# Kernel optimization log

Hardware: AMD Instinct MI355X
Metric: run time of the kernel (lower is better)

## Reference

```python
import jax, jax.numpy as jnp
import numpy as np

B = 128          # number of graphs
N = 512          # nodes per graph
D = 128          # input_dim == hid_dim
H = 128          # hid_dim
L = 2            # num GIN layers
E_PG = 8192      # edges per graph (avg degree 16)
OUT = 10
BN_EPS = 1e-5
RATIO = 0.5


def setup_inputs() -> dict:
    key = jax.random.key(0)
    ks = jax.random.split(key, 32)
    NT = B * N
    # per-graph random edges, offset into the global node index space
    e = jax.random.randint(ks[0], (2, B, E_PG), 0, N)
    offs = (jnp.arange(B) * N)[None, :, None]
    edge_index = (e + offs).reshape(2, -1).astype(jnp.int64)
    batch = jnp.repeat(jnp.arange(B), N).astype(jnp.int64)
    x = jax.random.normal(ks[1], (NT, D), dtype=jnp.float32)
    sc = 0.05
    inp = {
        'x': x, 'edge_index': edge_index, 'batch': batch,
        'epss': jax.random.normal(ks[2], (L,), jnp.float32) * 0.1,
        'Ws1': jax.random.normal(ks[3], (L, D, 2 * H), jnp.float32) * sc,
        'bs1': jax.random.normal(ks[4], (L, 2 * H), jnp.float32) * sc,
        'g1s': jax.random.uniform(ks[5], (L, 2 * H), jnp.float32, 0.5, 1.5),
        'be1s': jax.random.normal(ks[6], (L, 2 * H), jnp.float32) * sc,
        'rm1s': jax.random.normal(ks[7], (L, 2 * H), jnp.float32) * 0.1,
        'rv1s': jax.random.uniform(ks[8], (L, 2 * H), jnp.float32, 0.5, 1.5),
        'Ws2': jax.random.normal(ks[9], (L, 2 * H, H), jnp.float32) * sc,
        'bs2': jax.random.normal(ks[10], (L, H), jnp.float32) * sc,
        'gbn': jax.random.uniform(ks[11], (L, H), jnp.float32, 0.5, 1.5),
        'bbn': jax.random.normal(ks[12], (L, H), jnp.float32) * sc,
        'rmbn': jax.random.normal(ks[13], (L, H), jnp.float32) * 0.1,
        'rvbn': jax.random.uniform(ks[14], (L, H), jnp.float32, 0.5, 1.5),
        'Wrel': jax.random.normal(ks[15], (H, 1), jnp.float32) * sc,
        'brel': jax.random.normal(ks[16], (1,), jnp.float32) * sc,
        'Wroot': jax.random.normal(ks[17], (H, 1), jnp.float32) * sc,
        'W_lin1': jax.random.normal(ks[18], (H, H), jnp.float32) * sc,
        'b_lin1': jax.random.normal(ks[19], (H,), jnp.float32) * sc,
        'g_h': jax.random.uniform(ks[20], (H,), jnp.float32, 0.5, 1.5),
        'be_h': jax.random.normal(ks[21], (H,), jnp.float32) * sc,
        'rm_h': jax.random.normal(ks[22], (H,), jnp.float32) * 0.1,
        'rv_h': jax.random.uniform(ks[23], (H,), jnp.float32, 0.5, 1.5),
        'W_lin2': jax.random.normal(ks[24], (H, OUT), jnp.float32) * sc,
        'b_lin2': jax.random.normal(ks[25], (OUT,), jnp.float32) * sc,
    }
    return inp


def _bn(h, g, b, rm, rv):
    # eval-mode BatchNorm1d
    return (h - rm) * jax.lax.rsqrt(rv + BN_EPS) * g + b


def _forward(x, edge_index, batch, epss, Ws1, bs1, g1s, be1s, rm1s, rv1s,
             Ws2, bs2, gbn, bbn, rmbn, rvbn, Wrel, brel, Wroot,
             W_lin1, b_lin1, g_h, be_h, rm_h, rv_h, W_lin2, b_lin2):
    NT = x.shape[0]
    src, dst = edge_index[0], edge_index[1]
    # ---- stacked GINConv + BN + ReLU (eval: dropout = identity) ----
    for l in range(L):
        agg = jax.ops.segment_sum(x[src], dst, num_segments=NT)   # scatter-add
        h = (1.0 + epss[l]) * x + agg
        h = h @ Ws1[l] + bs1[l]
        h = jax.nn.relu(_bn(h, g1s[l], be1s[l], rm1s[l], rv1s[l]))
        h = h @ Ws2[l] + bs2[l]
        x = jax.nn.relu(_bn(h, gbn[l], bbn[l], rmbn[l], rvbn[l]))
    # ---- SAGPooling: GraphConv score -> tanh -> per-graph top-k ----
    agg = jax.ops.segment_sum(x[src], dst, num_segments=NT)
    score = (agg @ Wrel + brel + x @ Wroot)[:, 0]                 # [NT]
    s = jnp.tanh(score)
    K = int(np.ceil(RATIO * N))
    vals, idx = jax.lax.top_k(s.reshape(B, N), K)                 # [B,K]
    perm = (idx + (jnp.arange(B) * N)[:, None]).reshape(-1)       # global node ids
    x_pool = x[perm] * vals.reshape(-1)[:, None]                  # [B*K, H]
    batch_pool = batch[perm]
    # ---- global add pool ----
    embedding = jax.ops.segment_sum(x_pool, batch_pool, num_segments=B)  # [B,H]
    # ---- head (B > 1 branch) ----
    h = _bn(embedding @ W_lin1 + b_lin1, g_h, be_h, rm_h, rv_h)
    h = jax.nn.relu(h)
    logits = h @ W_lin2 + b_lin2
    return embedding, logits


def reference(x, edge_index, batch, epss, Ws1, bs1, g1s, be1s, rm1s, rv1s,
              Ws2, bs2, gbn, bbn, rmbn, rvbn, Wrel, brel, Wroot,
              W_lin1, b_lin1, g_h, be_h, rm_h, rv_h, W_lin2, b_lin2):
    return _forward(x, edge_index, batch, epss, Ws1, bs1, g1s, be1s, rm1s,
                    rv1s, Ws2, bs2, gbn, bbn, rmbn, rvbn, Wrel, brel, Wroot,
                    W_lin1, b_lin1, g_h, be_h, rm_h, rv_h, W_lin2, b_lin2)
```

## Files before the change

kernel.cpp:

```cpp
#include <hip/hip_runtime.h>
#include <hip/hip_bf16.h>
#include <stdint.h>
#include <math.h>

#define NT_ 65536
#define BGRAPH 128
#define NNODE 512
#define DIM 128
#define HID 128
#define H2 256
#define EDGES 1048576
#define EPG 8192
#define KSEL 256
#define OUTC 10

typedef float v2f __attribute__((ext_vector_type(2)));

__global__ __launch_bounds__(512) void k_csr(const int* __restrict__ src, const int* __restrict__ dst,
                                             int* __restrict__ row_start, int* __restrict__ csr2) {
    __shared__ int hist[512];
    __shared__ int scan_s[512];
    __shared__ int cur[512];
    __shared__ int eids[EPG];
    const int g = blockIdx.x;
    const int t = threadIdx.x;
    const int base = g * EPG;
    const int nb = g * NNODE;
    hist[t] = 0;
    __syncthreads();
    #pragma unroll
    for (int j = t; j < EPG; j += 512) {
        int d = dst[base + j] - nb;
        atomicAdd(&hist[d], 1);
    }
    __syncthreads();
    int v = hist[t];
    scan_s[t] = v;
    __syncthreads();
    for (int off = 1; off < 512; off <<= 1) {
        int u = (t >= off) ? scan_s[t - off] : 0;
        __syncthreads();
        scan_s[t] += u;
        __syncthreads();
    }
    int excl = scan_s[t] - v;
    row_start[nb + t] = base + excl;
    cur[t] = excl;
    if (g == BGRAPH - 1 && t == 511) row_start[NT_] = EDGES;
    __syncthreads();
    #pragma unroll
    for (int j = t; j < EPG; j += 512) {
        int d = dst[base + j] - nb;
        int pos = atomicAdd(&cur[d], 1);
        eids[pos] = (d << 16) | j;
    }
    __syncthreads();
    #pragma unroll
    for (int p = t; p < EPG; p += 512) {
        int packed = eids[p];
        int j = packed & 0xFFFF;
        int d = packed >> 16;
        int beg = scan_s[d] - hist[d];
        int end = scan_s[d];
        int rank = 0;
        for (int q = beg; q < end; ++q) rank += (int)((eids[q] & 0xFFFF) < j);
        csr2[base + beg + rank] = src[base + j];
    }
}

__global__ __launch_bounds__(256) void k_aggcomb(const float* __restrict__ X,
        const int* __restrict__ row_start, const int* __restrict__ csr_src,
        const float* __restrict__ epss, int l, float* __restrict__ XIN) {
    int bid = blockIdx.x;
    int wg = (bid & 7) * 1024 + (bid >> 3);
    int wave = threadIdx.x >> 6;
    int lane = threadIdx.x & 63;
    int half = lane >> 5;
    int l32 = lane & 31;
    int n = wg * 8 + wave * 2 + half;
    int beg = row_start[n], end = row_start[n + 1];
    const size_t co = (size_t)(l32 * 4);
    const float ep = __fadd_rn(1.0f, epss[l]);
    float a0 = 0.f, a1 = 0.f, a2 = 0.f, a3 = 0.f;
    int p = beg;
    for (; p + 8 <= end; p += 8) {
        int n0 = csr_src[p+0], n1 = csr_src[p+1], n2 = csr_src[p+2], n3 = csr_src[p+3];
        int n4 = csr_src[p+4], n5 = csr_src[p+5], n6 = csr_src[p+6], n7 = csr_src[p+7];
        float4 v0 = *(const float4*)(X + (size_t)n0 * DIM + co);
        float4 v1 = *(const float4*)(X + (size_t)n1 * DIM + co);
        float4 v2 = *(const float4*)(X + (size_t)n2 * DIM + co);
        float4 v3 = *(const float4*)(X + (size_t)n3 * DIM + co);
        float4 v4 = *(const float4*)(X + (size_t)n4 * DIM + co);
        float4 v5 = *(const float4*)(X + (size_t)n5 * DIM + co);
        float4 v6 = *(const float4*)(X + (size_t)n6 * DIM + co);
        float4 v7 = *(const float4*)(X + (size_t)n7 * DIM + co);
        a0 = __fadd_rn(a0, v0.x); a1 = __fadd_rn(a1, v0.y); a2 = __fadd_rn(a2, v0.z); a3 = __fadd_rn(a3, v0.w);
        a0 = __fadd_rn(a0, v1.x); a1 = __fadd_rn(a1, v1.y); a2 = __fadd_rn(a2, v1.z); a3 = __fadd_rn(a3, v1.w);
        a0 = __fadd_rn(a0, v2.x); a1 = __fadd_rn(a1, v2.y); a2 = __fadd_rn(a2, v2.z); a3 = __fadd_rn(a3, v2.w);
        a0 = __fadd_rn(a0, v3.x); a1 = __fadd_rn(a1, v3.y); a2 = __fadd_rn(a2, v3.z); a3 = __fadd_rn(a3, v3.w);
        a0 = __fadd_rn(a0, v4.x); a1 = __fadd_rn(a1, v4.y); a2 = __fadd_rn(a2, v4.z); a3 = __fadd_rn(a3, v4.w);
        a0 = __fadd_rn(a0, v5.x); a1 = __fadd_rn(a1, v5.y); a2 = __fadd_rn(a2, v5.z); a3 = __fadd_rn(a3, v5.w);
        a0 = __fadd_rn(a0, v6.x); a1 = __fadd_rn(a1, v6.y); a2 = __fadd_rn(a2, v6.z); a3 = __fadd_rn(a3, v6.w);
        a0 = __fadd_rn(a0, v7.x); a1 = __fadd_rn(a1, v7.y); a2 = __fadd_rn(a2, v7.z); a3 = __fadd_rn(a3, v7.w);
    }
    for (; p < end; ++p) {
        int nbr = csr_src[p];
        float4 v = *(const float4*)(X + (size_t)nbr * DIM + co);
        a0 = __fadd_rn(a0, v.x); a1 = __fadd_rn(a1, v.y); a2 = __fadd_rn(a2, v.z); a3 = __fadd_rn(a3, v.w);
    }
    float4 xv = *(const float4*)(X + (size_t)n * DIM + co);
    float4 o;
    o.x = __fadd_rn(__fmul_rn(ep, xv.x), a0);
    o.y = __fadd_rn(__fmul_rn(ep, xv.y), a1);
    o.z = __fadd_rn(__fmul_rn(ep, xv.z), a2);
    o.w = __fadd_rn(__fmul_rn(ep, xv.w), a3);
    *(float4*)(XIN + (size_t)n * DIM + co) = o;
}

__global__ __launch_bounds__(256) void k_gemm1(const float* __restrict__ XIN,
        const float* __restrict__ Ws1, const float* __restrict__ bs1,
        const float* __restrict__ g1s, const float* __restrict__ be1s, const float* __restrict__ rm1s,
        const float* __restrict__ rv1s, int l, float* __restrict__ H1out) {
    __shared__ float As[2][16][132];
    __shared__ float Bs[2][16][132];
    const float* W1  = Ws1 + (size_t)l * DIM * H2;
    const float* b1  = bs1 + l * H2;
    const float* g1  = g1s + l * H2;
    const float* be1 = be1s + l * H2;
    const float* rm1 = rm1s + l * H2;
    const float* rv1 = rv1s + l * H2;
    int bid = blockIdx.x;
    int wg = (bid & 7) * 128 + (bid >> 3);
    const int mbase = (wg >> 1) * 128;
    const int nbase = (wg & 1) * 128;
    const int tid = threadIdx.x;
    const int srow = tid >> 1;
    const int sk   = (tid & 1) * 8;
    const int bk   = tid >> 4;
    const int bc   = (tid & 15) * 4;
    const int ty = tid >> 4;
    const int tx = tid & 15;
    v2f acc[8][4] = {};
    const float* xr = XIN + (size_t)(mbase + srow) * DIM + sk;
    float4 px0, px1, pw0, pw1;
    px0 = *(const float4*)(xr);     px1 = *(const float4*)(xr + 4);
    {
        const float* wrow = W1 + (size_t)bk * H2 + nbase;
        pw0 = *(const float4*)(wrow + bc); pw1 = *(const float4*)(wrow + bc + 64);
    }
    As[0][sk + 0][srow] = px0.x;
    As[0][sk + 1][srow] = px0.y;
    As[0][sk + 2][srow] = px0.z;
    As[0][sk + 3][srow] = px0.w;
    As[0][sk + 4][srow] = px1.x;
    As[0][sk + 5][srow] = px1.y;
    As[0][sk + 6][srow] = px1.z;
    As[0][sk + 7][srow] = px1.w;
    *(float4*)&Bs[0][bk][bc]      = pw0;
    *(float4*)&Bs[0][bk][bc + 64] = pw1;
    __syncthreads();
    int cur = 0;
    for (int kt = 0; kt < DIM; kt += 16) {
        const int nxt = kt + 16;
        if (nxt < DIM) {
            px0 = *(const float4*)(xr + nxt);     px1 = *(const float4*)(xr + nxt + 4);
            const float* wrow = W1 + (size_t)(nxt + bk) * H2 + nbase;
            pw0 = *(const float4*)(wrow + bc); pw1 = *(const float4*)(wrow + bc + 64);
        }
        #pragma unroll
        for (int kk = 0; kk < 16; ++kk) {
            const float4 aA = *(const float4*)&As[cur][kk][ty * 8];
            const float4 aB = *(const float4*)&As[cur][kk][ty * 8 + 4];
            const float4 b0 = *(const float4*)&Bs[cur][kk][tx * 4];
            const float4 b1v = *(const float4*)&Bs[cur][kk][tx * 4 + 64];
            v2f b00; b00[0] = b0.x;  b00[1] = b0.y;
            v2f b01; b01[0] = b0.z;  b01[1] = b0.w;
            v2f b10; b10[0] = b1v.x; b10[1] = b1v.y;
            v2f b11; b11[0] = b1v.z; b11[1] = b1v.w;
            const float arr[8] = {aA.x, aA.y, aA.z, aA.w, aB.x, aB.y, aB.z, aB.w};
            #pragma unroll
            for (int i = 0; i < 8; ++i) {
                v2f ai; ai[0] = arr[i]; ai[1] = arr[i];
                acc[i][0] = __builtin_elementwise_fma(ai, b00, acc[i][0]);
                acc[i][1] = __builtin_elementwise_fma(ai, b01, acc[i][1]);
                acc[i][2] = __builtin_elementwise_fma(ai, b10, acc[i][2]);
                acc[i][3] = __builtin_elementwise_fma(ai, b11, acc[i][3]);
            }
        }
        if (nxt < DIM) {
            const int nb = cur ^ 1;
            As[nb][sk + 0][srow] = px0.x;
            As[nb][sk + 1][srow] = px0.y;
            As[nb][sk + 2][srow] = px0.z;
            As[nb][sk + 3][srow] = px0.w;
            As[nb][sk + 4][srow] = px1.x;
            As[nb][sk + 5][srow] = px1.y;
            As[nb][sk + 6][srow] = px1.z;
            As[nb][sk + 7][srow] = px1.w;
            *(float4*)&Bs[nb][bk][bc]      = pw0;
            *(float4*)&Bs[nb][bk][bc + 64] = pw1;
            __syncthreads();
        }
        cur ^= 1;
    }
    const int gc = nbase + tx * 4;
    float bb[8], iv[8], gg[8], rr[8], ee[8];
    #pragma unroll
    for (int j = 0; j < 8; ++j) {
        int c = (j < 4) ? (gc + j) : (gc + 60 + j);
        bb[j] = b1[c];
        iv[j] = __fdiv_rn(1.0f, __fsqrt_rn(__fadd_rn(rv1[c], 1e-5f)));
        gg[j] = g1[c];
        rr[j] = rm1[c];
        ee[j] = be1[c];
    }
    #pragma unroll
    for (int i = 0; i < 8; ++i) {
        const int gr = mbase + ty * 8 + i;
        float cv[8] = {acc[i][0][0], acc[i][0][1], acc[i][1][0], acc[i][1][1],
                       acc[i][2][0], acc[i][2][1], acc[i][3][0], acc[i][3][1]};
        float r[8];
        #pragma unroll
        for (int j = 0; j < 8; ++j) {
            float t = __fadd_rn(cv[j], bb[j]);
            t = __fsub_rn(t, rr[j]); t = __fmul_rn(t, iv[j]);
            t = __fmul_rn(t, gg[j]); t = __fadd_rn(t, ee[j]);
            r[j] = fmaxf(t, 0.f);
        }
        float4 o0; o0.x = r[0]; o0.y = r[1]; o0.z = r[2]; o0.w = r[3];
        float4 o1; o1.x = r[4]; o1.y = r[5]; o1.z = r[6]; o1.w = r[7];
        *(float4*)(H1out + (size_t)gr * H2 + gc)      = o0;
        *(float4*)(H1out + (size_t)gr * H2 + gc + 64) = o1;
    }
}

__global__ __launch_bounds__(256) void k_gemm2(const float* __restrict__ H1, const float* __restrict__ Ws2,
        const float* __restrict__ bs2, const float* __restrict__ gbn, const float* __restrict__ bbn,
        const float* __restrict__ rmbn, const float* __restrict__ rvbn, int l, float* __restrict__ Xout) {
    __shared__ float As[2][16][132];
    __shared__ float Bs[2][16][132];
    const float* W2 = Ws2 + (size_t)l * H2 * HID;
    const float* b2 = bs2 + l * HID;
    const float* g  = gbn + l * HID;
    const float* be = bbn + l * HID;
    const float* rm = rmbn + l * HID;
    const float* rv = rvbn + l * HID;
    int bid = blockIdx.x;
    int wg = (bid & 7) * 64 + (bid >> 3);
    const int mbase = wg * 128;
    const int tid = threadIdx.x;
    const int srow = tid >> 1;
    const int sk   = (tid & 1) * 8;
    const int bk   = tid >> 4;
    const int bc   = (tid & 15) * 4;
    const int ty = tid >> 4;
    const int tx = tid & 15;
    v2f acc[8][4] = {};
    const float* hr = H1 + (size_t)(mbase + srow) * H2 + sk;
    float4 ph0, ph1, pw0, pw1;
    ph0 = *(const float4*)(hr);     ph1 = *(const float4*)(hr + 4);
    {
        const float* wrow = W2 + (size_t)bk * HID;
        pw0 = *(const float4*)(wrow + bc); pw1 = *(const float4*)(wrow + bc + 64);
    }
    As[0][sk + 0][srow] = ph0.x;
    As[0][sk + 1][srow] = ph0.y;
    As[0][sk + 2][srow] = ph0.z;
    As[0][sk + 3][srow] = ph0.w;
    As[0][sk + 4][srow] = ph1.x;
    As[0][sk + 5][srow] = ph1.y;
    As[0][sk + 6][srow] = ph1.z;
    As[0][sk + 7][srow] = ph1.w;
    *(float4*)&Bs[0][bk][bc]      = pw0;
    *(float4*)&Bs[0][bk][bc + 64] = pw1;
    __syncthreads();
    int cur = 0;
    for (int kt = 0; kt < H2; kt += 16) {
        const int nxt = kt + 16;
        if (nxt < H2) {
            ph0 = *(const float4*)(hr + nxt);     ph1 = *(const float4*)(hr + nxt + 4);
            const float* wrow = W2 + (size_t)(nxt + bk) * HID;
            pw0 = *(const float4*)(wrow + bc); pw1 = *(const float4*)(wrow + bc + 64);
        }
        #pragma unroll
        for (int kk = 0; kk < 16; ++kk) {
            const float4 aA = *(const float4*)&As[cur][kk][ty * 8];
            const float4 aB = *(const float4*)&As[cur][kk][ty * 8 + 4];
            const float4 b0 = *(const float4*)&Bs[cur][kk][tx * 4];
            const float4 b1v = *(const float4*)&Bs[cur][kk][tx * 4 + 64];
            v2f b00; b00[0] = b0.x;  b00[1] = b0.y;
            v2f b01; b01[0] = b0.z;  b01[1] = b0.w;
            v2f b10; b10[0] = b1v.x; b10[1] = b1v.y;
            v2f b11; b11[0] = b1v.z; b11[1] = b1v.w;
            const float arr[8] = {aA.x, aA.y, aA.z, aA.w, aB.x, aB.y, aB.z, aB.w};
            #pragma unroll
            for (int i = 0; i < 8; ++i) {
                v2f ai; ai[0] = arr[i]; ai[1] = arr[i];
                acc[i][0] = __builtin_elementwise_fma(ai, b00, acc[i][0]);
                acc[i][1] = __builtin_elementwise_fma(ai, b01, acc[i][1]);
                acc[i][2] = __builtin_elementwise_fma(ai, b10, acc[i][2]);
                acc[i][3] = __builtin_elementwise_fma(ai, b11, acc[i][3]);
            }
        }
        if (nxt < H2) {
            const int nb = cur ^ 1;
            As[nb][sk + 0][srow] = ph0.x;
            As[nb][sk + 1][srow] = ph0.y;
            As[nb][sk + 2][srow] = ph0.z;
            As[nb][sk + 3][srow] = ph0.w;
            As[nb][sk + 4][srow] = ph1.x;
            As[nb][sk + 5][srow] = ph1.y;
            As[nb][sk + 6][srow] = ph1.z;
            As[nb][sk + 7][srow] = ph1.w;
            *(float4*)&Bs[nb][bk][bc]      = pw0;
            *(float4*)&Bs[nb][bk][bc + 64] = pw1;
            __syncthreads();
        }
        cur ^= 1;
    }
    const int gc = tx * 4;
    float bb[8], iv[8], gg[8], rr[8], ee[8];
    #pragma unroll
    for (int j = 0; j < 8; ++j) {
        int c = (j < 4) ? (gc + j) : (gc + 60 + j);
        bb[j] = b2[c];
        iv[j] = __fdiv_rn(1.0f, __fsqrt_rn(__fadd_rn(rv[c], 1e-5f)));
        gg[j] = g[c];
        rr[j] = rm[c];
        ee[j] = be[c];
    }
    #pragma unroll
    for (int i = 0; i < 8; ++i) {
        const int gr = mbase + ty * 8 + i;
        float cv[8] = {acc[i][0][0], acc[i][0][1], acc[i][1][0], acc[i][1][1],
                       acc[i][2][0], acc[i][2][1], acc[i][3][0], acc[i][3][1]};
        float r[8];
        #pragma unroll
        for (int j = 0; j < 8; ++j) {
            float t = __fadd_rn(cv[j], bb[j]);
            t = __fsub_rn(t, rr[j]); t = __fmul_rn(t, iv[j]);
            t = __fmul_rn(t, gg[j]); t = __fadd_rn(t, ee[j]);
            r[j] = fmaxf(t, 0.f);
        }
        float4 o0; o0.x = r[0]; o0.y = r[1]; o0.z = r[2]; o0.w = r[3];
        float4 o1; o1.x = r[4]; o1.y = r[5]; o1.z = r[6]; o1.w = r[7];
        *(float4*)(Xout + (size_t)gr * HID + gc)      = o0;
        *(float4*)(Xout + (size_t)gr * HID + gc + 64) = o1;
    }
}

__global__ __launch_bounds__(256) void k_ydot(const float* __restrict__ X,
        const float* __restrict__ Wrel, const float* __restrict__ Wroot,
        float* __restrict__ Y, float* __restrict__ Z) {
    int wave = threadIdx.x >> 6;
    int lane = threadIdx.x & 63;
    int n = blockIdx.x * 4 + wave;
    const float2 xv = *(const float2*)(X + (size_t)n * HID + lane * 2);
    const float2 wr = *(const float2*)(Wrel + lane * 2);
    const float2 wo = *(const float2*)(Wroot + lane * 2);
    float p1 = __fmaf_rn(xv.y, wr.y, __fmul_rn(xv.x, wr.x));
    float p2 = __fmaf_rn(xv.y, wo.y, __fmul_rn(xv.x, wo.x));
    #pragma unroll
    for (int off = 1; off <= 32; off <<= 1) {
        p1 += __shfl_xor(p1, off);
        p2 += __shfl_xor(p2, off);
    }
    if (lane == 0) { Y[n] = p1; Z[n] = p2; }
}

__global__ __launch_bounds__(256) void k_scorelite(const float* __restrict__ Y, const float* __restrict__ Z,
        const int* __restrict__ row_start, const int* __restrict__ csr_src,
        const float* __restrict__ brel, float* __restrict__ S) {
    int n = blockIdx.x * 256 + threadIdx.x;
    int beg = row_start[n], end = row_start[n + 1];
    float p1 = 0.f;
    for (int p = beg; p < end; ++p) p1 = __fadd_rn(p1, Y[csr_src[p]]);
    float pp = __fadd_rn(__fadd_rn(p1, brel[0]), Z[n]);
    const float PC = 7.90531110763549805f;
    float s;
    if (pp >= PC)       s = 1.0f;
    else if (pp <= -PC) s = -1.0f;
    else                s = (float)tanh((double)pp);
    S[n] = s;
}

__global__ __launch_bounds__(512) void k_poolhead(const float* __restrict__ X, const float* __restrict__ S,
        const float* __restrict__ W1, const float* __restrict__ b1,
        const float* __restrict__ gh, const float* __restrict__ beh,
        const float* __restrict__ rmh, const float* __restrict__ rvh,
        const float* __restrict__ W2, const float* __restrict__ b2,
        float* __restrict__ EMB, float* __restrict__ LOGITS) {
    __shared__ unsigned key[512];
    __shared__ double w[512];
    __shared__ double red[4][128];
    __shared__ double embs[128];
    __shared__ double hbuf[128];
    const int b = blockIdx.x, tid = threadIdx.x;
    float v = S[b * NNODE + tid];
    unsigned u = __float_as_uint(v);
    unsigned o = (u & 0x80000000u) ? ~u : (u | 0x80000000u);
    key[tid] = o;
    __syncthreads();
    int rank = 0;
    for (int j = 0; j < NNODE; ++j) {
        unsigned kj = key[j];
        rank += (int)((kj > o) || (kj == o && j < tid));
    }
    w[tid] = (rank < KSEL) ? (double)v : 0.0;
    __syncthreads();
    const int jgrp = tid >> 7;
    const int col = tid & 127;
    double acc = 0.0;
    for (int i = jgrp; i < NNODE; i += 4) {
        acc += (double)X[((size_t)b * NNODE + i) * HID + col] * w[i];
    }
    red[jgrp][col] = acc;
    __syncthreads();
    if (jgrp == 0) {
        double e = red[0][col] + red[1][col] + red[2][col] + red[3][col];
        EMB[b * HID + col] = (float)e;
        embs[col] = e;
    }
    __syncthreads();
    if (tid < 128) {
        double a = 0.0;
        for (int k = 0; k < HID; ++k) a += embs[k] * (double)W1[k * HID + tid];
        a += (double)b1[tid];
        double inv = 1.0 / sqrt((double)rvh[tid] + 1e-5);
        a = (a - (double)rmh[tid]) * inv * (double)gh[tid] + (double)beh[tid];
        hbuf[tid] = fmax(a, 0.0);
    }
    __syncthreads();
    if (tid < OUTC) {
        double a2 = (double)b2[tid];
        for (int k = 0; k < HID; ++k) a2 += hbuf[k] * (double)W2[k * OUTC + tid];
        LOGITS[b * OUTC + tid] = (float)a2;
    }
}

extern "C" void kernel_launch(void* const* d_in, const int* in_sizes, int n_in,
                              void* d_out, int out_size, void* d_ws, size_t ws_size,
                              hipStream_t stream) {
    const float* x     = (const float*)d_in[0];
    const int*   edge  = (const int*)d_in[1];
    const int*   src   = edge;
    const int*   dst   = edge + EDGES;
    const float* epss  = (const float*)d_in[3];
    const float* Ws1   = (const float*)d_in[4];
    const float* bs1   = (const float*)d_in[5];
    const float* g1s   = (const float*)d_in[6];
    const float* be1s  = (const float*)d_in[7];
    const float* rm1s  = (const float*)d_in[8];
    const float* rv1s  = (const float*)d_in[9];
    const float* Ws2   = (const float*)d_in[10];
    const float* bs2   = (const float*)d_in[11];
    const float* gbn   = (const float*)d_in[12];
    const float* bbn   = (const float*)d_in[13];
    const float* rmbn  = (const float*)d_in[14];
    const float* rvbn  = (const float*)d_in[15];
    const float* Wrel  = (const float*)d_in[16];
    const float* brel  = (const float*)d_in[17];
    const float* Wroot = (const float*)d_in[18];
    const float* W_lin1= (const float*)d_in[19];
    const float* b_lin1= (const float*)d_in[20];
    const float* g_h   = (const float*)d_in[21];
    const float* be_h  = (const float*)d_in[22];
    const float* rm_h  = (const float*)d_in[23];
    const float* rv_h  = (const float*)d_in[24];
    const float* W_lin2= (const float*)d_in[25];
    const float* b_lin2= (const float*)d_in[26];

    char* ws = (char*)d_ws;
    float*  x_cur    = (float*) (ws);
    float*  xin      = (float*) (ws + 33554432);
    float*  h1       = (float*) (ws + 67108864);
    float*  s32      = (float*) (ws + 134217728);
    float*  ybuf     = (float*) (ws + 134479872);
    float*  zbuf     = (float*) (ws + 134742016);
    int*    row_start= (int*)   (ws + 135004160);
    int*    csr2     = (int*)   (ws + 135290880);

    float* emb    = (float*)d_out;
    float* logits = (float*)d_out + BGRAPH * HID;

    k_csr<<<BGRAPH, 512, 0, stream>>>(src, dst, row_start, csr2);

    k_aggcomb<<<NT_ / 8, 256, 0, stream>>>(x, row_start, csr2, epss, 0, xin);
    k_gemm1<<<1024, 256, 0, stream>>>(xin, Ws1, bs1, g1s, be1s, rm1s, rv1s, 0, h1);
    k_gemm2<<<512, 256, 0, stream>>>(h1, Ws2, bs2, gbn, bbn, rmbn, rvbn, 0, x_cur);
    k_aggcomb<<<NT_ / 8, 256, 0, stream>>>(x_cur, row_start, csr2, epss, 1, xin);
    k_gemm1<<<1024, 256, 0, stream>>>(xin, Ws1, bs1, g1s, be1s, rm1s, rv1s, 1, h1);
    k_gemm2<<<512, 256, 0, stream>>>(h1, Ws2, bs2, gbn, bbn, rmbn, rvbn, 1, x_cur);
    k_ydot<<<NT_ / 4, 256, 0, stream>>>(x_cur, Wrel, Wroot, ybuf, zbuf);
    k_scorelite<<<NT_ / 256, 256, 0, stream>>>(ybuf, zbuf, row_start, csr2, brel, s32);
    k_poolhead<<<BGRAPH, 512, 0, stream>>>(x_cur, s32, W_lin1, b_lin1, g_h, be_h, rm_h, rv_h,
                                           W_lin2, b_lin2, emb, logits);
}
```

Baseline: 387.8 us.

## Split pool-head into score+select, parallel weighted sum, and head kernels

Moves the top-k rank selection into the scoring kernel, with one block per graph. The weighted pooling sum is split across 512 blocks, each covering a quarter of a graph and writing double partial sums. A small head kernel then reduces the partials and runs the MLP. The goal is to spread the memory-bound pooling over more CUs than the previous 128-block kernel. The cost is an extra launch and a partial-sum buffer round trip, and the scoring now uses only 128 blocks.

```diff
diff --git a/kernel.cpp b/kernel.cpp
--- a/kernel.cpp
+++ b/kernel.cpp
@@ -368,10 +368,12 @@
     if (lane == 0) { Y[n] = p1; Z[n] = p2; }
 }
 
-__global__ __launch_bounds__(256) void k_scorelite(const float* __restrict__ Y, const float* __restrict__ Z,
+__global__ __launch_bounds__(512) void k_selscore(const float* __restrict__ Y, const float* __restrict__ Z,
         const int* __restrict__ row_start, const int* __restrict__ csr_src,
-        const float* __restrict__ brel, float* __restrict__ S) {
-    int n = blockIdx.x * 256 + threadIdx.x;
+        const float* __restrict__ brel, float* __restrict__ WSEL) {
+    __shared__ unsigned key[512];
+    const int b = blockIdx.x, t = threadIdx.x;
+    const int n = b * NNODE + t;
     int beg = row_start[n], end = row_start[n + 1];
     float p1 = 0.f;
     for (int p = beg; p < end; ++p) p1 = __fadd_rn(p1, Y[csr_src[p]]);
@@ -381,60 +383,65 @@
     if (pp >= PC)       s = 1.0f;
     else if (pp <= -PC) s = -1.0f;
     else                s = (float)tanh((double)pp);
-    S[n] = s;
-}
-
-__global__ __launch_bounds__(512) void k_poolhead(const float* __restrict__ X, const float* __restrict__ S,
+    unsigned u = __float_as_uint(s);
+    unsigned o = (u & 0x80000000u) ? ~u : (u | 0x80000000u);
+    key[t] = o;
+    __syncthreads();
+    int rank = 0;
+    for (int j = 0; j < NNODE; ++j) {
+        unsigned kj = key[j];
+        rank += (int)((kj > o) || (kj == o && j < t));
+    }
+    WSEL[n] = (rank < KSEL) ? s : 0.0f;
+}
+
+__global__ __launch_bounds__(256) void k_wsum(const float* __restrict__ X,
+        const float* __restrict__ WSEL, double* __restrict__ PB) {
+    __shared__ float wl[128];
+    const int blk = blockIdx.x;
+    const int g = blk >> 2, q = blk & 3;
+    const int t = threadIdx.x;
+    const int col = t & 127, half = t >> 7;
+    if (t < 128) wl[t] = WSEL[g * NNODE + q * 128 + t];
+    __syncthreads();
+    const int lr0 = half * 64;
+    const float* xb = X + ((size_t)(g * NNODE + q * 128 + lr0)) * HID + col;
+    double acc = 0.0;
+    #pragma unroll 4
+    for (int i = 0; i < 64; ++i) {
+        acc += (double)xb[(size_t)i * HID] * (double)wl[lr0 + i];
+    }
+    PB[((size_t)blk * 2 + half) * 128 + col] = acc;
+}
+
+__global__ __launch_bounds__(128) void k_headc(const double* __restrict__ PB,
         const float* __restrict__ W1, const float* __restrict__ b1,
         const float* __restrict__ gh, const float* __restrict__ beh,
         const float* __restrict__ rmh, const float* __restrict__ rvh,
         const float* __restrict__ W2, const float* __restrict__ b2,
         float* __restrict__ EMB, float* __restrict__ LOGITS) {
-    __shared__ unsigned key[512];
-    __shared__ double w[512];
-    __shared__ double red[4][128];
     __shared__ double embs[128];
     __shared__ double hbuf[128];
-    const int b = blockIdx.x, tid = threadIdx.x;
-    float v = S[b * NNODE + tid];
-    unsigned u = __float_as_uint(v);
-    unsigned o = (u & 0x80000000u) ? ~u : (u | 0x80000000u);
-    key[tid] = o;
-    __syncthreads();
-    int rank = 0;
-    for (int j = 0; j < NNODE; ++j) {
-        unsigned kj = key[j];
-        rank += (int)((kj > o) || (kj == o && j < tid));
-    }
-    w[tid] = (rank < KSEL) ? (double)v : 0.0;
-    __syncthreads();
-    const int jgrp = tid >> 7;
-    const int col = tid & 127;
-    double acc = 0.0;
-    for (int i = jgrp; i < NNODE; i += 4) {
-        acc += (double)X[((size_t)b * NNODE + i) * HID + col] * w[i];
-    }
-    red[jgrp][col] = acc;
-    __syncthreads();
-    if (jgrp == 0) {
-        double e = red[0][col] + red[1][col] + red[2][col] + red[3][col];
-        EMB[b * HID + col] = (float)e;
-        embs[col] = e;
-    }
-    __syncthreads();
-    if (tid < 128) {
-        double a = 0.0;
-        for (int k = 0; k < HID; ++k) a += embs[k] * (double)W1[k * HID + tid];
-        a += (double)b1[tid];
-        double inv = 1.0 / sqrt((double)rvh[tid] + 1e-5);
-        a = (a - (double)rmh[tid]) * inv * (double)gh[tid] + (double)beh[tid];
-        hbuf[tid] = fmax(a, 0.0);
-    }
-    __syncthreads();
-    if (tid < OUTC) {
-        double a2 = (double)b2[tid];
-        for (int k = 0; k < HID; ++k) a2 += hbuf[k] * (double)W2[k * OUTC + tid];
-        LOGITS[b * OUTC + tid] = (float)a2;
+    const int b = blockIdx.x, t = threadIdx.x;
+    double e = 0.0;
+    #pragma unroll
+    for (int part = 0; part < 8; ++part) {
+        e += PB[((size_t)(b * 4) * 2 + part) * 128 + t];
+    }
+    EMB[b * HID + t] = (float)e;
+    embs[t] = e;
+    __syncthreads();
+    double a = 0.0;
+    for (int k = 0; k < HID; ++k) a += embs[k] * (double)W1[k * HID + t];
+    a += (double)b1[t];
+    double inv = 1.0 / sqrt((double)rvh[t] + 1e-5);
+    a = (a - (double)rmh[t]) * inv * (double)gh[t] + (double)beh[t];
+    hbuf[t] = fmax(a, 0.0);
+    __syncthreads();
+    if (t < OUTC) {
+        double a2 = (double)b2[t];
+        for (int k = 0; k < HID; ++k) a2 += hbuf[k] * (double)W2[k * OUTC + t];
+        LOGITS[b * OUTC + t] = (float)a2;
     }
 }
 
@@ -474,11 +481,12 @@
     float*  x_cur    = (float*) (ws);
     float*  xin      = (float*) (ws + 33554432);
     float*  h1       = (float*) (ws + 67108864);
-    float*  s32      = (float*) (ws + 134217728);
+    float*  wsel     = (float*) (ws + 134217728);
     float*  ybuf     = (float*) (ws + 134479872);
     float*  zbuf     = (float*) (ws + 134742016);
-    int*    row_start= (int*)   (ws + 135004160);
-    int*    csr2     = (int*)   (ws + 135290880);
+    double* pbuf     = (double*)(ws + 135004160);
+    int*    row_start= (int*)   (ws + 136052736);
+    int*    csr2     = (int*)   (ws + 136339456);
 
     float* emb    = (float*)d_out;
     float* logits = (float*)d_out + BGRAPH * HID;
@@ -492,7 +500,8 @@
     k_gemm1<<<1024, 256, 0, stream>>>(xin, Ws1, bs1, g1s, be1s, rm1s, rv1s, 1, h1);
     k_gemm2<<<512, 256, 0, stream>>>(h1, Ws2, bs2, gbn, bbn, rmbn, rvbn, 1, x_cur);
     k_ydot<<<NT_ / 4, 256, 0, stream>>>(x_cur, Wrel, Wroot, ybuf, zbuf);
-    k_scorelite<<<NT_ / 256, 256, 0, stream>>>(ybuf, zbuf, row_start, csr2, brel, s32);
-    k_poolhead<<<BGRAPH, 512, 0, stream>>>(x_cur, s32, W_lin1, b_lin1, g_h, be_h, rm_h, rv_h,
-                                           W_lin2, b_lin2, emb, logits);
-}
+    k_selscore<<<BGRAPH, 512, 0, stream>>>(ybuf, zbuf, row_start, csr2, brel, wsel);
+    k_wsum<<<4 * BGRAPH, 256, 0, stream>>>(x_cur, wsel, pbuf);
+    k_headc<<<BGRAPH, 128, 0, stream>>>(pbuf, W_lin1, b_lin1, g_h, be_h, rm_h, rv_h,
+                                        W_lin2, b_lin2, emb, logits);
+}
```

Measured after the change: 367.1 us. 1.06x faster.
